# Kernel tuning notes

Measured on AMD Instinct MI355X. Metric: run time of the kernel, lower is better.

## Reference

```python
import jax, jax.numpy as jnp
import numpy as np


def setup_inputs() -> dict:
    key = jax.random.key(0)
    k1, k2 = jax.random.split(key)
    b, s, h = 32, 4096, 1024
    decoder_state_t = jax.random.normal(k1, (b, h), dtype=jnp.float32)
    encoder_outputs = jax.random.normal(k2, (b, s, h), dtype=jnp.float32)
    return {"decoder_state_t": decoder_state_t, "encoder_outputs": encoder_outputs}


def reference(decoder_state_t, encoder_outputs):
    # scores[b,s] = sum_h decoder_state_t[b,h] * encoder_outputs[b,s,h]
    scores = jnp.einsum("bh,bsh->bs", decoder_state_t, encoder_outputs)
    attn = jax.nn.softmax(scores, axis=-1)
    # context[b,h] = sum_s attn[b,s] * encoder_outputs[b,s,h]
    context = jnp.einsum("bs,bsh->bh", attn, encoder_outputs)
    return (context, attn)
```

## Files before the change

### kernel.cpp

```cpp
#include <hip/hip_runtime.h>
#include <math.h>

#define B 32
#define S 4096
#define H 1024
#define NCHUNK 32
#define ROWS_PER_BLOCK (S / NCHUNK)
#define ROWS_PER_WAVE (ROWS_PER_BLOCK/4)
#define PSTRIDE 1040

__global__ __launch_bounds__(256) void attn_pass1(
    const float* __restrict__ dec, const float* __restrict__ enc,
    float* __restrict__ scores, float* __restrict__ part)
{
    const int blk   = blockIdx.x;
    const int b     = blk / NCHUNK;
    const int chunk = blk % NCHUNK;
    const int lane  = threadIdx.x & 63;
    const int w     = threadIdx.x >> 6;

    const float4* dsp = (const float4*)(dec + (size_t)b * H);
    const float4 ds0 = dsp[lane];
    const float4 ds1 = dsp[lane + 64];
    const float4 ds2 = dsp[lane + 128];
    const float4 ds3 = dsp[lane + 192];

    float m = -INFINITY, l = 0.f;
    float4 a0 = {0.f,0.f,0.f,0.f}, a1 = a0, a2 = a0, a3 = a0;

    const int row0 = chunk * ROWS_PER_BLOCK + w * ROWS_PER_WAVE;
    for (int r = 0; r < ROWS_PER_WAVE; ++r) {
        const int row = row0 + r;
        const float4* ep = (const float4*)(enc + ((size_t)b * S + row) * H);
        const float4 e0 = ep[lane];
        const float4 e1 = ep[lane + 64];
        const float4 e2 = ep[lane + 128];
        const float4 e3 = ep[lane + 192];

        float p = 0.f;
        p = fmaf(e0.x, ds0.x, p); p = fmaf(e0.y, ds0.y, p);
        p = fmaf(e0.z, ds0.z, p); p = fmaf(e0.w, ds0.w, p);
        p = fmaf(e1.x, ds1.x, p); p = fmaf(e1.y, ds1.y, p);
        p = fmaf(e1.z, ds1.z, p); p = fmaf(e1.w, ds1.w, p);
        p = fmaf(e2.x, ds2.x, p); p = fmaf(e2.y, ds2.y, p);
        p = fmaf(e2.z, ds2.z, p); p = fmaf(e2.w, ds2.w, p);
        p = fmaf(e3.x, ds3.x, p); p = fmaf(e3.y, ds3.y, p);
        p = fmaf(e3.z, ds3.z, p); p = fmaf(e3.w, ds3.w, p);

        p += __shfl_xor(p, 32);
        p += __shfl_xor(p, 16);
        p += __shfl_xor(p, 8);
        p += __shfl_xor(p, 4);
        p += __shfl_xor(p, 2);
        p += __shfl_xor(p, 1);
        const float score = p;

        if (lane == 0) scores[(size_t)b * S + row] = score;

        if (score > m) {
            const float alpha = __expf(m - score);
            m = score;
            l = fmaf(l, alpha, 1.f);
            a0.x = fmaf(a0.x, alpha, e0.x); a0.y = fmaf(a0.y, alpha, e0.y);
            a0.z = fmaf(a0.z, alpha, e0.z); a0.w = fmaf(a0.w, alpha, e0.w);
            a1.x = fmaf(a1.x, alpha, e1.x); a1.y = fmaf(a1.y, alpha, e1.y);
            a1.z = fmaf(a1.z, alpha, e1.z); a1.w = fmaf(a1.w, alpha, e1.w);
            a2.x = fmaf(a2.x, alpha, e2.x); a2.y = fmaf(a2.y, alpha, e2.y);
            a2.z = fmaf(a2.z, alpha, e2.z); a2.w = fmaf(a2.w, alpha, e2.w);
            a3.x = fmaf(a3.x, alpha, e3.x); a3.y = fmaf(a3.y, alpha, e3.y);
            a3.z = fmaf(a3.z, alpha, e3.z); a3.w = fmaf(a3.w, alpha, e3.w);
        } else {
            const float pe = __expf(score - m);
            l += pe;
            a0.x = fmaf(pe, e0.x, a0.x); a0.y = fmaf(pe, e0.y, a0.y);
            a0.z = fmaf(pe, e0.z, a0.z); a0.w = fmaf(pe, e0.w, a0.w);
            a1.x = fmaf(pe, e1.x, a1.x); a1.y = fmaf(pe, e1.y, a1.y);
            a1.z = fmaf(pe, e1.z, a1.z); a1.w = fmaf(pe, e1.w, a1.w);
            a2.x = fmaf(pe, e2.x, a2.x); a2.y = fmaf(pe, e2.y, a2.y);
            a2.z = fmaf(pe, e2.z, a2.z); a2.w = fmaf(pe, e2.w, a2.w);
            a3.x = fmaf(pe, e3.x, a3.x); a3.y = fmaf(pe, e3.y, a3.y);
            a3.z = fmaf(pe, e3.z, a3.z); a3.w = fmaf(pe, e3.w, a3.w);
        }
    }

    __shared__ float sm[4], sl[4];
    __shared__ float sc[4][1024];
    if (lane == 0) { sm[w] = m; sl[w] = l; }
    *(float4*)&sc[w][lane * 4]       = a0;
    *(float4*)&sc[w][lane * 4 + 256] = a1;
    *(float4*)&sc[w][lane * 4 + 512] = a2;
    *(float4*)&sc[w][lane * 4 + 768] = a3;
    __syncthreads();

    const float M  = fmaxf(fmaxf(sm[0], sm[1]), fmaxf(sm[2], sm[3]));
    const float al0 = __expf(sm[0] - M), al1 = __expf(sm[1] - M);
    const float al2 = __expf(sm[2] - M), al3 = __expf(sm[3] - M);
    const float Lb = sl[0]*al0 + sl[1]*al1 + sl[2]*al2 + sl[3]*al3;

    const int t = threadIdx.x;
    const float4 c0 = *(const float4*)&sc[0][t * 4];
    const float4 c1 = *(const float4*)&sc[1][t * 4];
    const float4 c2 = *(const float4*)&sc[2][t * 4];
    const float4 c3 = *(const float4*)&sc[3][t * 4];
    float4 cp;
    cp.x = c0.x*al0 + c1.x*al1 + c2.x*al2 + c3.x*al3;
    cp.y = c0.y*al0 + c1.y*al1 + c2.y*al2 + c3.y*al3;
    cp.z = c0.z*al0 + c1.z*al1 + c2.z*al2 + c3.z*al3;
    cp.w = c0.w*al0 + c1.w*al1 + c2.w*al2 + c3.w*al3;

    float* pb = part + (size_t)blk * PSTRIDE;
    *(float4*)&pb[t * 4] = cp;
    if (t == 0) { pb[1024] = M; pb[1025] = Lb; }
}

__global__ __launch_bounds__(256) void attn_pass2(
    const float* __restrict__ scores, const float* __restrict__ part,
    float* __restrict__ out)
{
    const int b = blockIdx.x >> 2;
    const int j = blockIdx.x & 3;
    const int t = threadIdx.x;
    const float* pbase = part + (size_t)b * NCHUNK * PSTRIDE;

    float M = -INFINITY;
    for (int i = 0; i < NCHUNK; ++i)
        M = fmaxf(M, pbase[i * PSTRIDE + 1024]);
    float L = 0.f;
    for (int i = 0; i < NCHUNK; ++i)
        L += pbase[i * PSTRIDE + 1025] * __expf(pbase[i * PSTRIDE + 1024] - M);
    const float invL = 1.f / L;

    const int h = j * 256 + t;
    float acc = 0.f;
    for (int i = 0; i < NCHUNK; ++i)
        acc = fmaf(__expf(pbase[i * PSTRIDE + 1024] - M),
                   pbase[i * PSTRIDE + h], acc);
    out[(size_t)b * H + h] = acc * invL;

    float* attn_out = out + (size_t)B * H;
    for (int k = 0; k < 4; ++k) {
        const int s = j * 1024 + k * 256 + t;
        attn_out[(size_t)b * S + s] =
            __expf(scores[(size_t)b * S + s] - M) * invL;
    }
}

extern "C" void kernel_launch(void* const* d_in, const int* in_sizes, int n_in,
                              void* d_out, int out_size, void* d_ws, size_t ws_size,
                              hipStream_t stream) {
    const float* dec = (const float*)d_in[0];
    const float* enc = (const float*)d_in[1];
    float* out = (float*)d_out;
    float* ws  = (float*)d_ws;
    float* scores = ws;
    float* part   = ws + (size_t)B * S;

    attn_pass1<<<B * NCHUNK, 256, 0, stream>>>(dec, enc, scores, part);
    attn_pass2<<<B * 4, 256, 0, stream>>>(scores, part, out);
}
```

Before: 687.1 us.

## Double-buffer encoder row-pair loads and batch online-softmax updates per pair

The pass-1 loop now processes encoder rows in pairs, using two sets of registers so the next pair's global loads are issued before the current pair is consumed. The two row dot products and their wave reductions are interleaved, the running max is rescaled once per pair instead of branching per row, and the score writes are merged into one float2 store. This aims to hide memory latency in a bandwidth-bound streaming kernel and cut serial shuffle and branch overhead. The cost is much higher register pressure (32 extra fx4 values in flight), which could lower occupancy.

```diff
diff --git a/kernel.cpp b/kernel.cpp
--- a/kernel.cpp
+++ b/kernel.cpp
@@ -7,7 +7,71 @@
 #define NCHUNK 32
 #define ROWS_PER_BLOCK (S / NCHUNK)
 #define ROWS_PER_WAVE (ROWS_PER_BLOCK/4)
+#define NPAIRS (ROWS_PER_WAVE/2)
 #define PSTRIDE 1040
+
+typedef float fx4 __attribute__((ext_vector_type(4)));
+
+__device__ __forceinline__ float dot16(const fx4 e0, const fx4 e1,
+                                       const fx4 e2, const fx4 e3,
+                                       const fx4 d0, const fx4 d1,
+                                       const fx4 d2, const fx4 d3)
+{
+    float pa = e0.x * d0.x;
+    pa = fmaf(e0.y, d0.y, pa); pa = fmaf(e0.z, d0.z, pa); pa = fmaf(e0.w, d0.w, pa);
+    pa = fmaf(e1.x, d1.x, pa); pa = fmaf(e1.y, d1.y, pa);
+    pa = fmaf(e1.z, d1.z, pa); pa = fmaf(e1.w, d1.w, pa);
+    float pb = e2.x * d2.x;
+    pb = fmaf(e2.y, d2.y, pb); pb = fmaf(e2.z, d2.z, pb); pb = fmaf(e2.w, d2.w, pb);
+    pb = fmaf(e3.x, d3.x, pb); pb = fmaf(e3.y, d3.y, pb);
+    pb = fmaf(e3.z, d3.z, pb); pb = fmaf(e3.w, d3.w, pb);
+    return pa + pb;
+}
+
+__device__ __forceinline__ fx4 fma4(const float s, const fx4 v, fx4 acc) {
+    acc.x = fmaf(s, v.x, acc.x); acc.y = fmaf(s, v.y, acc.y);
+    acc.z = fmaf(s, v.z, acc.z); acc.w = fmaf(s, v.w, acc.w);
+    return acc;
+}
+
+#define LOAD_PAIR(E0, E1, E2, E3, E4, E5, E6, E7, ROW)                        \
+    do {                                                                      \
+        const fx4* ep0_ = (const fx4*)(enc_b + (size_t)(ROW) * H);            \
+        const fx4* ep1_ = (const fx4*)(enc_b + (size_t)((ROW) + 1) * H);      \
+        E0 = ep0_[lane];       E1 = ep0_[lane + 64];                          \
+        E2 = ep0_[lane + 128]; E3 = ep0_[lane + 192];                         \
+        E4 = ep1_[lane];       E5 = ep1_[lane + 64];                          \
+        E6 = ep1_[lane + 128]; E7 = ep1_[lane + 192];                         \
+    } while (0)
+
+#define CONSUME_PAIR(E0, E1, E2, E3, E4, E5, E6, E7, ROW)                     \
+    do {                                                                      \
+        float p0 = dot16(E0, E1, E2, E3, ds0, ds1, ds2, ds3);                 \
+        float p1 = dot16(E4, E5, E6, E7, ds0, ds1, ds2, ds3);                 \
+        _Pragma("unroll")                                                     \
+        for (int st_ = 32; st_ >= 1; st_ >>= 1) {                             \
+            p0 += __shfl_xor(p0, st_);                                        \
+            p1 += __shfl_xor(p1, st_);                                        \
+        }                                                                     \
+        if (lane == 0) {                                                      \
+            float2 sv_ = {p0, p1};                                            \
+            *(float2*)(scores + (size_t)b * S + (ROW)) = sv_;                 \
+        }                                                                     \
+        const float gm_ = fmaxf(p0, p1);                                      \
+        if (gm_ > m) {                               \
+            const float alpha_ = __expf(m - gm_); \
+            m = gm_;                                                          \
+            l *= alpha_;                                                      \
+            a0 *= alpha_; a1 *= alpha_; a2 *= alpha_; a3 *= alpha_;           \
+        }                                                                     \
+        const float w0_ = __expf(p0 - m);                                     \
+        const float w1_ = __expf(p1 - m);                                     \
+        l += w0_ + w1_;                                                       \
+        a0 = fma4(w0_, E0, fma4(w1_, E4, a0));                                \
+        a1 = fma4(w0_, E1, fma4(w1_, E5, a1));                                \
+        a2 = fma4(w0_, E2, fma4(w1_, E6, a2));                                \
+        a3 = fma4(w0_, E3, fma4(w1_, E7, a3));                                \
+    } while (0)
 
 __global__ __launch_bounds__(256) void attn_pass1(
     const float* __restrict__ dec, const float* __restrict__ enc,
@@ -19,97 +83,58 @@
     const int lane  = threadIdx.x & 63;
     const int w     = threadIdx.x >> 6;
 
-    const float4* dsp = (const float4*)(dec + (size_t)b * H);
-    const float4 ds0 = dsp[lane];
-    const float4 ds1 = dsp[lane + 64];
-    const float4 ds2 = dsp[lane + 128];
-    const float4 ds3 = dsp[lane + 192];
+    const fx4* dsp = (const fx4*)(dec + (size_t)b * H);
+    const fx4 ds0 = dsp[lane];
+    const fx4 ds1 = dsp[lane + 64];
+    const fx4 ds2 = dsp[lane + 128];
+    const fx4 ds3 = dsp[lane + 192];
 
     float m = -INFINITY, l = 0.f;
-    float4 a0 = {0.f,0.f,0.f,0.f}, a1 = a0, a2 = a0, a3 = a0;
+    fx4 a0 = {0.f, 0.f, 0.f, 0.f}, a1 = a0, a2 = a0, a3 = a0;
 
     const int row0 = chunk * ROWS_PER_BLOCK + w * ROWS_PER_WAVE;
-    for (int r = 0; r < ROWS_PER_WAVE; ++r) {
-        const int row = row0 + r;
-        const float4* ep = (const float4*)(enc + ((size_t)b * S + row) * H);
-        const float4 e0 = ep[lane];
-        const float4 e1 = ep[lane + 64];
-        const float4 e2 = ep[lane + 128];
-        const float4 e3 = ep[lane + 192];
+    const float* enc_b = enc + (size_t)b * S * H;
 
-        float p = 0.f;
-        p = fmaf(e0.x, ds0.x, p); p = fmaf(e0.y, ds0.y, p);
-        p = fmaf(e0.z, ds0.z, p); p = fmaf(e0.w, ds0.w, p);
-        p = fmaf(e1.x, ds1.x, p); p = fmaf(e1.y, ds1.y, p);
-        p = fmaf(e1.z, ds1.z, p); p = fmaf(e1.w, ds1.w, p);
-        p = fmaf(e2.x, ds2.x, p); p = fmaf(e2.y, ds2.y, p);
-        p = fmaf(e2.z, ds2.z, p); p = fmaf(e2.w, ds2.w, p);
-        p = fmaf(e3.x, ds3.x, p); p = fmaf(e3.y, ds3.y, p);
-        p = fmaf(e3.z, ds3.z, p); p = fmaf(e3.w, ds3.w, p);
+    fx4 eA0, eA1, eA2, eA3, eA4, eA5, eA6, eA7;
+    fx4 eB0, eB1, eB2, eB3, eB4, eB5, eB6, eB7;
 
-        p += __shfl_xor(p, 32);
-        p += __shfl_xor(p, 16);
-        p += __shfl_xor(p, 8);
-        p += __shfl_xor(p, 4);
-        p += __shfl_xor(p, 2);
-        p += __shfl_xor(p, 1);
-        const float score = p;
+    LOAD_PAIR(eA0, eA1, eA2, eA3, eA4, eA5, eA6, eA7, row0);
 
-        if (lane == 0) scores[(size_t)b * S + row] = score;
+    for (int p = 0; p < NPAIRS; p += 2) {
+        const int rowA = row0 + p * 2;
+        const int rowB = rowA + 2;
+        LOAD_PAIR(eB0, eB1, eB2, eB3, eB4, eB5, eB6, eB7, rowB);
+        CONSUME_PAIR(eA0, eA1, eA2, eA3, eA4, eA5, eA6, eA7, rowA);
 
-        if (score > m) {
-            const float alpha = __expf(m - score);
-            m = score;
-            l = fmaf(l, alpha, 1.f);
-            a0.x = fmaf(a0.x, alpha, e0.x); a0.y = fmaf(a0.y, alpha, e0.y);
-            a0.z = fmaf(a0.z, alpha, e0.z); a0.w = fmaf(a0.w, alpha, e0.w);
-            a1.x = fmaf(a1.x, alpha, e1.x); a1.y = fmaf(a1.y, alpha, e1.y);
-            a1.z = fmaf(a1.z, alpha, e1.z); a1.w = fmaf(a1.w, alpha, e1.w);
-            a2.x = fmaf(a2.x, alpha, e2.x); a2.y = fmaf(a2.y, alpha, e2.y);
-            a2.z = fmaf(a2.z, alpha, e2.z); a2.w = fmaf(a2.w, alpha, e2.w);
-            a3.x = fmaf(a3.x, alpha, e3.x); a3.y = fmaf(a3.y, alpha, e3.y);
-            a3.z = fmaf(a3.z, alpha, e3.z); a3.w = fmaf(a3.w, alpha, e3.w);
-        } else {
-            const float pe = __expf(score - m);
-            l += pe;
-            a0.x = fmaf(pe, e0.x, a0.x); a0.y = fmaf(pe, e0.y, a0.y);
-            a0.z = fmaf(pe, e0.z, a0.z); a0.w = fmaf(pe, e0.w, a0.w);
-            a1.x = fmaf(pe, e1.x, a1.x); a1.y = fmaf(pe, e1.y, a1.y);
-            a1.z = fmaf(pe, e1.z, a1.z); a1.w = fmaf(pe, e1.w, a1.w);
-            a2.x = fmaf(pe, e2.x, a2.x); a2.y = fmaf(pe, e2.y, a2.y);
-            a2.z = fmaf(pe, e2.z, a2.z); a2.w = fmaf(pe, e2.w, a2.w);
-            a3.x = fmaf(pe, e3.x, a3.x); a3.y = fmaf(pe, e3.y, a3.y);
-            a3.z = fmaf(pe, e3.z, a3.z); a3.w = fmaf(pe, e3.w, a3.w);
+        if (p + 2 < NPAIRS) {
+            LOAD_PAIR(eA0, eA1, eA2, eA3, eA4, eA5, eA6, eA7, rowB + 2);
         }
+        CONSUME_PAIR(eB0, eB1, eB2, eB3, eB4, eB5, eB6, eB7, rowB);
     }
 
     __shared__ float sm[4], sl[4];
     __shared__ float sc[4][1024];
     if (lane == 0) { sm[w] = m; sl[w] = l; }
-    *(float4*)&sc[w][lane * 4]       = a0;
-    *(float4*)&sc[w][lane * 4 + 256] = a1;
-    *(float4*)&sc[w][lane * 4 + 512] = a2;
-    *(float4*)&sc[w][lane * 4 + 768] = a3;
+    *(fx4*)&sc[w][lane * 4]       = a0;
+    *(fx4*)&sc[w][lane * 4 + 256] = a1;
+    *(fx4*)&sc[w][lane * 4 + 512] = a2;
+    *(fx4*)&sc[w][lane * 4 + 768] = a3;
     __syncthreads();
 
-    const float M  = fmaxf(fmaxf(sm[0], sm[1]), fmaxf(sm[2], sm[3]));
+    const float M   = fmaxf(fmaxf(sm[0], sm[1]), fmaxf(sm[2], sm[3]));
     const float al0 = __expf(sm[0] - M), al1 = __expf(sm[1] - M);
     const float al2 = __expf(sm[2] - M), al3 = __expf(sm[3] - M);
-    const float Lb = sl[0]*al0 + sl[1]*al1 + sl[2]*al2 + sl[3]*al3;
+    const float Lb  = sl[0] * al0 + sl[1] * al1 + sl[2] * al2 + sl[3] * al3;
 
     const int t = threadIdx.x;
-    const float4 c0 = *(const float4*)&sc[0][t * 4];
-    const float4 c1 = *(const float4*)&sc[1][t * 4];
-    const float4 c2 = *(const float4*)&sc[2][t * 4];
-    const float4 c3 = *(const float4*)&sc[3][t * 4];
-    float4 cp;
-    cp.x = c0.x*al0 + c1.x*al1 + c2.x*al2 + c3.x*al3;
-    cp.y = c0.y*al0 + c1.y*al1 + c2.y*al2 + c3.y*al3;
-    cp.z = c0.z*al0 + c1.z*al1 + c2.z*al2 + c3.z*al3;
-    cp.w = c0.w*al0 + c1.w*al1 + c2.w*al2 + c3.w*al3;
+    const fx4 c0 = *(const fx4*)&sc[0][t * 4];
+    const fx4 c1 = *(const fx4*)&sc[1][t * 4];
+    const fx4 c2 = *(const fx4*)&sc[2][t * 4];
+    const fx4 c3 = *(const fx4*)&sc[3][t * 4];
+    const fx4 cp = c0 * al0 + c1 * al1 + c2 * al2 + c3 * al3;
 
     float* pb = part + (size_t)blk * PSTRIDE;
-    *(float4*)&pb[t * 4] = cp;
+    *(fx4*)&pb[t * 4] = cp;
     if (t == 0) { pb[1024] = M; pb[1025] = Lb; }
 }
 
```

New measurement: 680.2 us. About the same (-1.0%).
